# Performance work log

Hardware: AMD Instinct MI355X
Metric: run time of the kernel (lower is better)

The kernel has to match this reference:

```python
import jax, jax.numpy as jnp
import numpy as np

N = 200000          # num nodes (num_rus)
E = 12800000        # num edges (avg degree 64)
IN_C, HID, OUT = 1, 16, 4


def setup_inputs() -> dict:
    key = jax.random.key(0)
    ks = jax.random.split(key, 6)
    x = jax.random.normal(ks[0], (N, IN_C), dtype=jnp.float32)
    edges = jax.random.randint(ks[1], (2, E), 0, N, dtype=jnp.int64)
    W1 = jax.random.normal(ks[2], (IN_C, HID), dtype=jnp.float32) / np.sqrt(IN_C)
    b1 = jnp.zeros((HID,), dtype=jnp.float32)
    W2 = jax.random.normal(ks[3], (HID, HID), dtype=jnp.float32) / np.sqrt(HID)
    b2 = jnp.zeros((HID,), dtype=jnp.float32)
    Wl = jax.random.normal(ks[4], (HID, OUT), dtype=jnp.float32) / np.sqrt(HID)
    bl = jnp.zeros((OUT,), dtype=jnp.float32)
    return {"x": x, "edges": edges, "W1": W1, "b1": b1, "W2": W2, "b2": b2, "Wl": Wl, "bl": bl}


def _gcn_norm(edges):
    # PyG GCNConv default: add self-loops, symmetric normalization.
    loops = jnp.arange(N, dtype=edges.dtype)
    src = jnp.concatenate([edges[0], loops])   # [E+N]
    dst = jnp.concatenate([edges[1], loops])
    deg = jax.ops.segment_sum(jnp.ones_like(dst, dtype=jnp.float32), dst, num_segments=N)
    dinv = jnp.where(deg > 0, jax.lax.rsqrt(deg), 0.0)
    norm = dinv[src] * dinv[dst]               # [E+N]
    return src, dst, norm


def _gcn_conv(h, W, b, src, dst, norm):
    m = h @ W                                  # [N, out] transform first (cheap, small C)
    msgs = m[src] * norm[:, None]              # gather + normalize, [E+N, out]
    agg = jax.ops.segment_sum(msgs, dst, num_segments=N)
    return agg + b


def reference(x, edges, W1, b1, W2, b2, Wl, bl):
    src, dst, norm = _gcn_norm(edges)
    h = jax.nn.relu(_gcn_conv(x, W1, b1, src, dst, norm))
    h = jax.nn.relu(_gcn_conv(h, W2, b2, src, dst, norm))
    return h @ Wl + bl                         # [N, 4]
```

## Files before the change

### kernel.cpp

```cpp
#include <hip/hip_runtime.h>

#define HID 16
#define OUTC 4
#define G 64
#define SBSH 8
#define SBN 256
#define CAP 21504
#define PHSH 15
#define SUBK 8
#define KB (SBN * SUBK)
#define PBLK 512
#define NPB_MAX 800
#define STCAP 32
#define STP 33
#define EPP (PBLK * 4)
#define SENT 0xFFFFFFFFu

__device__ __forceinline__ float relu(float v) { return v > 0.f ? v : 0.f; }

__global__ void k_cnt(const int* __restrict__ dst, int* __restrict__ cnt,
                      int E, int nsb, int nc, int ncsh) {
    __shared__ int lc[NPB_MAX];
    for (int i = threadIdx.x; i < nsb; i += PBLK) lc[i] = 0;
    __syncthreads();
    int c = blockIdx.x;
    int chunk = (E + nc - 1) / nc;
    int lo = c * chunk, hi = lo + chunk < E ? lo + chunk : E;
    for (int i = lo + threadIdx.x; i < hi; i += PBLK)
        atomicAdd(lc + (dst[i] >> SBSH), 1);
    __syncthreads();
    for (int b = threadIdx.x; b < nsb; b += PBLK)
        cnt[(b << ncsh) + c] = (lc[b] + 15) & ~15;
}

__global__ void k_scanA(int* __restrict__ a, int* __restrict__ bsum, int L) {
    __shared__ int s[1024];
    int i = blockIdx.x * 1024 + threadIdx.x;
    int v = (i < L) ? a[i] : 0;
    s[threadIdx.x] = v; __syncthreads();
    for (int off = 1; off < 1024; off <<= 1) {
        int t = (threadIdx.x >= (unsigned)off) ? s[threadIdx.x - off] : 0;
        __syncthreads();
        s[threadIdx.x] += t;
        __syncthreads();
    }
    if (i < L) a[i] = s[threadIdx.x] - v;
    if (threadIdx.x == 1023) bsum[blockIdx.x] = s[1023];
}

__global__ void k_scanB(int* __restrict__ bsum, int SB) {
    __shared__ int s[1024];
    int carry = 0;
    for (int base = 0; base < SB; base += 1024) {
        int idx = base + threadIdx.x;
        int v = (idx < SB) ? bsum[idx] : 0;
        s[threadIdx.x] = v; __syncthreads();
        for (int off = 1; off < 1024; off <<= 1) {
            int t = (threadIdx.x >= (unsigned)off) ? s[threadIdx.x - off] : 0;
            __syncthreads();
            s[threadIdx.x] += t;
            __syncthreads();
        }
        if (idx < SB) bsum[idx] = carry + s[threadIdx.x] - v;
        carry += s[1023];
        __syncthreads();
    }
    if (threadIdx.x == 0) bsum[SB] = carry;
}

__global__ void k_scanC(int* __restrict__ a, const int* __restrict__ bsum,
                        int* __restrict__ bOff, int L, int nsb, int SB,
                        int nc, int ncsh) {
    int i = blockIdx.x * 1024 + threadIdx.x;
    if (i < L) {
        int v = a[i] + bsum[blockIdx.x];
        a[i] = v;
        if ((i & (nc - 1)) == 0) bOff[i >> ncsh] = v;
    }
    if (blockIdx.x == 0 && threadIdx.x == 0) bOff[nsb] = bsum[SB];
}

__global__ void __launch_bounds__(PBLK) k_part(const int* __restrict__ src,
                                               const int* __restrict__ dst,
                                               const int* __restrict__ cnt,
                                               unsigned int* __restrict__ rec,
                                               int E, int nsb, int nc, int ncsh) {
    __shared__ unsigned int stage[NPB_MAX * STP];
    __shared__ int scnt[NPB_MAX];
    __shared__ int gcur[NPB_MAX];
    int c = blockIdx.x;
    for (int b = threadIdx.x; b < nsb; b += PBLK) {
        scnt[b] = 0;
        gcur[b] = cnt[(b << ncsh) + c];
    }
    __syncthreads();
    int chunk = (E + nc - 1) / nc;
    int lo = c * chunk, hi = lo + chunk < E ? lo + chunk : E;
    for (int base = lo; base < hi; base += EPP) {
#pragma unroll
        for (int k = 0; k < 4; ++k) {
            int i = base + k * PBLK + threadIdx.x;
            if (i < hi) {
                int d = dst[i], s = src[i];
                int b = d >> SBSH;
                int pos = atomicAdd(scnt + b, 1);
                if (pos < STCAP)
                    stage[b * STP + pos] = (unsigned int)s | ((unsigned int)(d & (SBN - 1)) << 18);
            }
        }
        __syncthreads();
        for (int b = threadIdx.x; b < nsb; b += PBLK) {
            int n = scnt[b];
            int f = n & ~15;
            if (f > 0) {
                uint4* d4 = (uint4*)&rec[gcur[b]];
                const unsigned int* sp0 = &stage[b * STP];
                for (int j = 0; j < f; j += 16) {
                    const unsigned int* sp = sp0 + j;
                    d4[0] = make_uint4(sp[0], sp[1], sp[2], sp[3]);
                    d4[1] = make_uint4(sp[4], sp[5], sp[6], sp[7]);
                    d4[2] = make_uint4(sp[8], sp[9], sp[10], sp[11]);
                    d4[3] = make_uint4(sp[12], sp[13], sp[14], sp[15]);
                    d4 += 4;
                }
                gcur[b] += f;
                for (int j = 0; j < n - f; ++j) stage[b * STP + j] = stage[b * STP + f + j];
                scnt[b] = n - f;
            }
        }
        __syncthreads();
    }
    for (int b = threadIdx.x; b < nsb; b += PBLK) {
        int n = scnt[b];
        if (n > 0) {
            unsigned int tmp[16];
            for (int j = 0; j < 16; ++j) tmp[j] = (j < n) ? stage[b * STP + j] : SENT;
            uint4* d4 = (uint4*)&rec[gcur[b]];
            d4[0] = make_uint4(tmp[0], tmp[1], tmp[2], tmp[3]);
            d4[1] = make_uint4(tmp[4], tmp[5], tmp[6], tmp[7]);
            d4[2] = make_uint4(tmp[8], tmp[9], tmp[10], tmp[11]);
            d4[3] = make_uint4(tmp[12], tmp[13], tmp[14], tmp[15]);
        }
    }
}

__global__ void __launch_bounds__(256) k_sort(const int* __restrict__ bOff,
                                              unsigned int* __restrict__ rec,
                                              float* __restrict__ dinv,
                                              int* __restrict__ rowp,
                                              int N, int nsb, int E) {
    __shared__ unsigned int raw[CAP];
    __shared__ int hist[KB], cur[KB];
    __shared__ int s[256];
    int b = blockIdx.x;
    int beg = bOff[b], end = bOff[b + 1];
    int size = end - beg; if (size > CAP) size = CAP;
    for (int i = threadIdx.x; i < size; i += 256) raw[i] = rec[beg + i];
    for (int k = threadIdx.x; k < KB; k += 256) hist[k] = 0;
    __syncthreads();
    for (int i = threadIdx.x; i < size; i += 256) {
        unsigned int r = raw[i];
        if (r == SENT) continue;
        int key = (int)((r >> 18) << 3) | (int)((r & 0x3FFFF) >> PHSH);
        atomicAdd(hist + key, 1);
    }
    __syncthreads();
    int t = threadIdx.x;
    int psum = 0;
#pragma unroll
    for (int j = 0; j < SUBK; ++j) psum += hist[t * SUBK + j];
    s[t] = psum; __syncthreads();
    for (int off = 1; off < 256; off <<= 1) {
        int v = (t >= off) ? s[t - off] : 0;
        __syncthreads();
        s[t] += v;
        __syncthreads();
    }
    int ex = s[t] - psum;
    {
        int n = b * SBN + t;
        bool valid = (n < N);
        int running = ex;
#pragma unroll
        for (int j = 0; j < SUBK; ++j) {
            cur[t * SUBK + j] = running;
            if (valid) rowp[(size_t)n * SUBK + j] = beg + running;
            running += hist[t * SUBK + j];
        }
        if (valid) dinv[n] = rsqrtf((float)psum + 1.0f);
    }
    __syncthreads();
    for (int i = t; i < size; i += 256) {
        unsigned int r = raw[i];
        if (r == SENT) continue;
        int key = (int)((r >> 18) << 3) | (int)((r & 0x3FFFF) >> PHSH);
        int p = atomicAdd(cur + key, 1);
        rec[beg + p] = r & 0x3FFFF;
    }
}

__global__ void k_m1(const float* __restrict__ x, const float* __restrict__ W1,
                     const float* __restrict__ dinv, float* __restrict__ m, int N) {
    int t = blockIdx.x * blockDim.x + threadIdx.x;
    if (t < N * HID) {
        int n = t >> 4, c = t & 15;
        m[t] = x[n] * W1[c] * dinv[n];
    }
}

__global__ void k_m2(float4* __restrict__ h4, const float* __restrict__ W2,
                     const float* __restrict__ dinv, int N) {
    __shared__ float hs[64][HID + 1];
    __shared__ float w[HID * HID];
    if (threadIdx.x < HID * HID) w[threadIdx.x] = W2[threadIdx.x];
    int idx = blockIdx.x * 256 + threadIdx.x;
    int n = idx >> 2, q = idx & 3;
    int ln = threadIdx.x >> 2;
    if (n < N) {
        float4 v = h4[idx];
        hs[ln][q * 4 + 0] = v.x; hs[ln][q * 4 + 1] = v.y;
        hs[ln][q * 4 + 2] = v.z; hs[ln][q * 4 + 3] = v.w;
    }
    __syncthreads();
    if (n < N) {
        float dn = dinv[n];
        float4 acc = make_float4(0.f, 0.f, 0.f, 0.f);
        const float* hr = hs[ln];
#pragma unroll
        for (int ci = 0; ci < HID; ++ci) {
            float hv = hr[ci];
            const float* wr = w + ci * HID + q * 4;
            acc.x += hv * wr[0]; acc.y += hv * wr[1];
            acc.z += hv * wr[2]; acc.w += hv * wr[3];
        }
        acc.x *= dn; acc.y *= dn; acc.z *= dn; acc.w *= dn;
        h4[idx] = acc;
    }
}

template <int MODE>
__global__ void __launch_bounds__(256) k_aggp(const int* __restrict__ rowp,
                                              const unsigned int* __restrict__ adj,
                                              const float* __restrict__ dinv,
                                              const float4* __restrict__ mS4,
                                              float4* __restrict__ gagg4,
                                              const float4* __restrict__ b4,
                                              const float* __restrict__ Wl,
                                              const float* __restrict__ bl,
                                              float* __restrict__ out,
                                              int N, int p) {
    __shared__ float hs[G][HID + 1];
    __shared__ float wl[HID * OUTC];
    __shared__ float blv[OUTC];
    if (MODE == 2) {
        if (threadIdx.x < HID * OUTC) wl[threadIdx.x] = Wl[threadIdx.x];
        if (threadIdx.x < OUTC) blv[threadIdx.x] = bl[threadIdx.x];
    }
    int dl = threadIdx.x >> 2, q = threadIdx.x & 3;
    int n = blockIdx.x * G + dl;
    if (n < N) {
        int i = rowp[(size_t)n * SUBK + p];
        int end = rowp[(size_t)n * SUBK + p + 1];
        float4 acc = (p == 0) ? mS4[n * 4 + q] : gagg4[n * 4 + q];
        for (; i + 4 <= end; i += 4) {
            int s0 = adj[i] * 4 + q, s1 = adj[i + 1] * 4 + q;
            int s2 = adj[i + 2] * 4 + q, s3 = adj[i + 3] * 4 + q;
            float4 v0 = mS4[s0], v1 = mS4[s1], v2 = mS4[s2], v3 = mS4[s3];
            acc.x += v0.x + v1.x + v2.x + v3.x;
            acc.y += v0.y + v1.y + v2.y + v3.y;
            acc.z += v0.z + v1.z + v2.z + v3.z;
            acc.w += v0.w + v1.w + v2.w + v3.w;
        }
        for (; i < end; ++i) {
            float4 v = mS4[adj[i] * 4 + q];
            acc.x += v.x; acc.y += v.y; acc.z += v.z; acc.w += v.w;
        }
        if (MODE == 0) {
            gagg4[n * 4 + q] = acc;
        } else {
            float dn = dinv[n];
            float4 bb = b4[q];
            float4 h;
            h.x = relu(acc.x * dn + bb.x);
            h.y = relu(acc.y * dn + bb.y);
            h.z = relu(acc.z * dn + bb.z);
            h.w = relu(acc.w * dn + bb.w);
            if (MODE == 1) {
                gagg4[n * 4 + q] = h;
            } else {
                hs[dl][q * 4 + 0] = h.x; hs[dl][q * 4 + 1] = h.y;
                hs[dl][q * 4 + 2] = h.z; hs[dl][q * 4 + 3] = h.w;
            }
        }
    }
    if (MODE == 2) {
        __syncthreads();
        if (n < N) {
            float acc = blv[q];
            const float* hr = hs[dl];
#pragma unroll
            for (int ci = 0; ci < HID; ++ci) acc += hr[ci] * wl[ci * OUTC + q];
            out[n * OUTC + q] = acc;
        }
    }
}

static inline size_t alignup(size_t v, size_t a) { return (v + a - 1) & ~(a - 1); }

extern "C" void kernel_launch(void* const* d_in, const int* in_sizes, int n_in,
                              void* d_out, int out_size, void* d_ws, size_t ws_size,
                              hipStream_t stream) {
    const float* x  = (const float*)d_in[0];
    const int* ed   = (const int*)d_in[1];
    const float* W1 = (const float*)d_in[2];
    const float* b1 = (const float*)d_in[3];
    const float* W2 = (const float*)d_in[4];
    const float* b2 = (const float*)d_in[5];
    const float* Wl = (const float*)d_in[6];
    const float* bl = (const float*)d_in[7];
    float* out      = (float*)d_out;

    int N = in_sizes[0];
    int E = in_sizes[1] / 2;
    const int* src = ed;
    const int* dst = ed + E;
    int nsb = (N + SBN - 1) / SBN;
    int nb64 = (N + G - 1) / G;
    int nphase = (N + (1 << PHSH) - 1) >> PHSH;

    int nc = 256, ncsh = 8;
    size_t o = 0;
    float* dinv; int* rowp; int* bsum; int* bOff; unsigned int* rec;
    float* bufA; float* bufB;
    char* w = (char*)d_ws;
    for (int attempt = 0; attempt < 2; ++attempt) {
        int L = nsb * nc;
        int SB = (L + 1023) / 1024;
        size_t Epad = (size_t)E + 15 * (size_t)L;
        o = 0;
        dinv = (float*)(w + o); o = alignup(o + (size_t)N * 4, 64);
        rowp = (int*)(w + o);   o = alignup(o + (size_t)N * SUBK * 4, 64);
        bsum = (int*)(w + o);   o = alignup(o + ((size_t)SB + 1) * 4, 64);
        bOff = (int*)(w + o);   o = alignup(o + ((size_t)nsb + 1) * 4, 64);
        rec  = (unsigned int*)(w + o); o = alignup(o + Epad * 4, 64);
        bufA = (float*)(w + o); o = alignup(o + (size_t)N * HID * 4, 64);
        bufB = (float*)(w + o); o = alignup(o + (size_t)N * HID * 4, 64);
        if (o <= ws_size || nc == 128) break;
        nc = 128; ncsh = 7;
    }
    int L = nsb * nc;
    int SB = (L + 1023) / 1024;
    int* cnt = (int*)bufA;

    int blk = 256;
    int gN16 = (N * HID + blk - 1) / blk;

    k_cnt<<<nc, PBLK, 0, stream>>>(dst, cnt, E, nsb, nc, ncsh);
    k_scanA<<<SB, 1024, 0, stream>>>(cnt, bsum, L);
    k_scanB<<<1, 1024, 0, stream>>>(bsum, SB);
    k_scanC<<<SB, 1024, 0, stream>>>(cnt, bsum, bOff, L, nsb, SB, nc, ncsh);
    k_part<<<nc, PBLK, 0, stream>>>(src, dst, cnt, rec, E, nsb, nc, ncsh);
    k_sort<<<nsb, 256, 0, stream>>>(bOff, rec, dinv, rowp, N, nsb, E);

    k_m1<<<gN16, blk, 0, stream>>>(x, W1, dinv, bufA, N);
    for (int p = 0; p < nphase; ++p) {
        if (p < nphase - 1)
            k_aggp<0><<<nb64, blk, 0, stream>>>(rowp, rec, dinv, (const float4*)bufA,
                                                (float4*)bufB, (const float4*)b1,
                                                nullptr, nullptr, nullptr, N, p);
        else
            k_aggp<1><<<nb64, blk, 0, stream>>>(rowp, rec, dinv, (const float4*)bufA,
                                                (float4*)bufB, (const float4*)b1,
                                                nullptr, nullptr, nullptr, N, p);
    }

    k_m2<<<nb64, blk, 0, stream>>>((float4*)bufB, W2, dinv, N);
    for (int p = 0; p < nphase; ++p) {
        if (p < nphase - 1)
            k_aggp<0><<<nb64, blk, 0, stream>>>(rowp, rec, dinv, (const float4*)bufB,
                                                (float4*)bufA, (const float4*)b2,
                                                nullptr, nullptr, nullptr, N, p);
        else
            k_aggp<2><<<nb64, blk, 0, stream>>>(rowp, rec, dinv, (const float4*)bufB,
                                                (float4*)bufA, (const float4*)b2,
                                                Wl, bl, out, N, p);
    }
}
```

Measured before the change: 567.5 us.

## Split partition and count kernels across two blocks per chunk by bucket parity

Each edge chunk is now handled by two blocks, each owning only the even or odd destination super-buckets. This halves the shared staging, counter and cursor arrays per block, so more blocks can be resident, and doubles the grid for k_cnt and k_part. The staging capacity per bucket is raised slightly, and PHSH is changed as well. The cost is that every block reads the full src/dst chunk, so index reads from global memory double for these kernels.

```diff
diff --git a/kernel.cpp b/kernel.cpp
--- a/kernel.cpp
+++ b/kernel.cpp
@@ -6,13 +6,13 @@
 #define SBSH 8
 #define SBN 256
 #define CAP 21504
-#define PHSH 15
+#define PHSH 16
 #define SUBK 8
 #define KB (SBN * SUBK)
 #define PBLK 512
-#define NPB_MAX 800
-#define STCAP 32
-#define STP 33
+#define NPB_H 400
+#define STCAP 34
+#define STP 35
 #define EPP (PBLK * 4)
 #define SENT 0xFFFFFFFFu
 
@@ -20,17 +20,20 @@
 
 __global__ void k_cnt(const int* __restrict__ dst, int* __restrict__ cnt,
                       int E, int nsb, int nc, int ncsh) {
-    __shared__ int lc[NPB_MAX];
-    for (int i = threadIdx.x; i < nsb; i += PBLK) lc[i] = 0;
-    __syncthreads();
-    int c = blockIdx.x;
+    __shared__ int lc[NPB_H];
+    int c = blockIdx.x >> 1, h = blockIdx.x & 1;
+    int nh = (nsb - h + 1) >> 1;
+    for (int i = threadIdx.x; i < nh; i += PBLK) lc[i] = 0;
+    __syncthreads();
     int chunk = (E + nc - 1) / nc;
     int lo = c * chunk, hi = lo + chunk < E ? lo + chunk : E;
-    for (int i = lo + threadIdx.x; i < hi; i += PBLK)
-        atomicAdd(lc + (dst[i] >> SBSH), 1);
-    __syncthreads();
-    for (int b = threadIdx.x; b < nsb; b += PBLK)
-        cnt[(b << ncsh) + c] = (lc[b] + 15) & ~15;
+    for (int i = lo + threadIdx.x; i < hi; i += PBLK) {
+        int b = dst[i] >> SBSH;
+        if ((b & 1) == h) atomicAdd(lc + (b >> 1), 1);
+    }
+    __syncthreads();
+    for (int bh = threadIdx.x; bh < nh; bh += PBLK)
+        cnt[((bh * 2 + h) << ncsh) + c] = (lc[bh] + 15) & ~15;
 }
 
 __global__ void k_scanA(int* __restrict__ a, int* __restrict__ bsum, int L) {
@@ -85,13 +88,14 @@
                                                const int* __restrict__ cnt,
                                                unsigned int* __restrict__ rec,
                                                int E, int nsb, int nc, int ncsh) {
-    __shared__ unsigned int stage[NPB_MAX * STP];
-    __shared__ int scnt[NPB_MAX];
-    __shared__ int gcur[NPB_MAX];
-    int c = blockIdx.x;
-    for (int b = threadIdx.x; b < nsb; b += PBLK) {
-        scnt[b] = 0;
-        gcur[b] = cnt[(b << ncsh) + c];
+    __shared__ unsigned int stage[NPB_H * STP];
+    __shared__ int scnt[NPB_H];
+    __shared__ int gcur[NPB_H];
+    int c = blockIdx.x >> 1, h = blockIdx.x & 1;
+    int nh = (nsb - h + 1) >> 1;
+    for (int bh = threadIdx.x; bh < nh; bh += PBLK) {
+        scnt[bh] = 0;
+        gcur[bh] = cnt[((bh * 2 + h) << ncsh) + c];
     }
     __syncthreads();
     int chunk = (E + nc - 1) / nc;
@@ -103,18 +107,21 @@
             if (i < hi) {
                 int d = dst[i], s = src[i];
                 int b = d >> SBSH;
-                int pos = atomicAdd(scnt + b, 1);
-                if (pos < STCAP)
-                    stage[b * STP + pos] = (unsigned int)s | ((unsigned int)(d & (SBN - 1)) << 18);
+                if ((b & 1) == h) {
+                    int bh = b >> 1;
+                    int pos = atomicAdd(scnt + bh, 1);
+                    if (pos < STCAP)
+                        stage[bh * STP + pos] = (unsigned int)s | ((unsigned int)(d & (SBN - 1)) << 18);
+                }
             }
         }
         __syncthreads();
-        for (int b = threadIdx.x; b < nsb; b += PBLK) {
-            int n = scnt[b];
+        for (int bh = threadIdx.x; bh < nh; bh += PBLK) {
+            int n = scnt[bh];
             int f = n & ~15;
             if (f > 0) {
-                uint4* d4 = (uint4*)&rec[gcur[b]];
-                const unsigned int* sp0 = &stage[b * STP];
+                uint4* d4 = (uint4*)&rec[gcur[bh]];
+                const unsigned int* sp0 = &stage[bh * STP];
                 for (int j = 0; j < f; j += 16) {
                     const unsigned int* sp = sp0 + j;
                     d4[0] = make_uint4(sp[0], sp[1], sp[2], sp[3]);
@@ -123,19 +130,19 @@
                     d4[3] = make_uint4(sp[12], sp[13], sp[14], sp[15]);
                     d4 += 4;
                 }
-                gcur[b] += f;
-                for (int j = 0; j < n - f; ++j) stage[b * STP + j] = stage[b * STP + f + j];
-                scnt[b] = n - f;
+                gcur[bh] += f;
+                for (int j = 0; j < n - f; ++j) stage[bh * STP + j] = stage[bh * STP + f + j];
+                scnt[bh] = n - f;
             }
         }
         __syncthreads();
     }
-    for (int b = threadIdx.x; b < nsb; b += PBLK) {
-        int n = scnt[b];
+    for (int bh = threadIdx.x; bh < nh; bh += PBLK) {
+        int n = scnt[bh];
         if (n > 0) {
             unsigned int tmp[16];
-            for (int j = 0; j < 16; ++j) tmp[j] = (j < n) ? stage[b * STP + j] : SENT;
-            uint4* d4 = (uint4*)&rec[gcur[b]];
+            for (int j = 0; j < 16; ++j) tmp[j] = (j < n) ? stage[bh * STP + j] : SENT;
+            uint4* d4 = (uint4*)&rec[gcur[bh]];
             d4[0] = make_uint4(tmp[0], tmp[1], tmp[2], tmp[3]);
             d4[1] = make_uint4(tmp[4], tmp[5], tmp[6], tmp[7]);
             d4[2] = make_uint4(tmp[8], tmp[9], tmp[10], tmp[11]);
@@ -355,11 +362,11 @@
     int blk = 256;
     int gN16 = (N * HID + blk - 1) / blk;
 
-    k_cnt<<<nc, PBLK, 0, stream>>>(dst, cnt, E, nsb, nc, ncsh);
+    k_cnt<<<nc * 2, PBLK, 0, stream>>>(dst, cnt, E, nsb, nc, ncsh);
     k_scanA<<<SB, 1024, 0, stream>>>(cnt, bsum, L);
     k_scanB<<<1, 1024, 0, stream>>>(bsum, SB);
     k_scanC<<<SB, 1024, 0, stream>>>(cnt, bsum, bOff, L, nsb, SB, nc, ncsh);
-    k_part<<<nc, PBLK, 0, stream>>>(src, dst, cnt, rec, E, nsb, nc, ncsh);
+    k_part<<<nc * 2, PBLK, 0, stream>>>(src, dst, cnt, rec, E, nsb, nc, ncsh);
     k_sort<<<nsb, 256, 0, stream>>>(bOff, rec, dinv, rowp, N, nsb, E);
 
     k_m1<<<gN16, blk, 0, stream>>>(x, W1, dinv, bufA, N);
```

After: 571.0 us. Within noise of the previous version (+0.6%).
